# Kernel tuning notes

Measured on AMD Instinct MI355X. Metric: run time of the kernel, lower is better.

Reference implementation:

```python
import jax, jax.numpy as jnp
import numpy as np

KEEP_RATIO = 0.7

def setup_inputs() -> dict:
    key = jax.random.key(0)
    k1, k2, k3 = jax.random.split(key, 3)
    B, N, D = 4, 16384, 1024
    H = D // 4
    x = jax.random.normal(k1, (B, N, D), dtype=jnp.float32)
    W1 = jax.random.normal(k2, (D, H), dtype=jnp.float32) * (1.0 / np.sqrt(D))
    b1 = jnp.zeros((H,), dtype=jnp.float32)
    W2 = jax.random.normal(k3, (H, 1), dtype=jnp.float32) * (1.0 / np.sqrt(H))
    b2 = jnp.zeros((1,), dtype=jnp.float32)
    return {"x": x, "W1": W1, "b1": b1, "W2": W2, "b2": b2}

def reference(x, W1, b1, W2, b2):
    # x: [B, N, D]
    B, N, D = x.shape
    k = int(N * KEEP_RATIO)  # static under jit
    h = jax.nn.relu(jnp.einsum('bnd,dh->bnh', x, W1) + b1)
    scores = jax.nn.sigmoid(jnp.einsum('bnh,ho->bno', h, W2) + b2)  # [B, N, 1]
    score_values = scores[..., 0]  # [B, N]
    x_weighted = x * scores  # [B, N, D]
    _, top_k_indices = jax.lax.top_k(score_values, k)  # [B, k]
    top_k_indices = jnp.sort(top_k_indices, axis=1)
    x_kept = jnp.take_along_axis(x_weighted, top_k_indices[:, :, None], axis=1)  # [B, k, D]
    sparsity_loss = -jnp.mean(jnp.abs(score_values - 0.5))
    return x_kept, sparsity_loss
```

## Files before the change

### kernel.cpp

```cpp
#include <hip/hip_runtime.h>
#include <hip/hip_bf16.h>
#include <math.h>

#define N_TOK 16384
#define BATCH 4
#define DIM   1024
#define HID   256
#define KEEP  11468
#define MROWS 65536
#define BK    32
#define NKT   (DIM / BK)
#define DELTA 6e-3f
#define WCAP  4096
#define AP    40
#define ASLOT (128 * AP)
#define BSLOT (16 * 512)

typedef __attribute__((ext_vector_type(8))) short bf16x8;
typedef __attribute__((ext_vector_type(4))) float f32x4;

__device__ inline unsigned bf16_rne(float f) {
    unsigned u = __float_as_uint(f);
    return (u + 0x7FFFu + ((u >> 16) & 1u)) >> 16;
}

#define GLDS16(gp, lp) __builtin_amdgcn_global_load_lds( \
    (const __attribute__((address_space(1))) void*)(gp), \
    (__attribute__((address_space(3))) void*)(lp), 16, 0, 0)

__global__ __launch_bounds__(256) void prep_kernel(
    const float* __restrict__ W1, ushort* __restrict__ Wpk)
{
    const int kt = blockIdx.x;
    for (int idx = threadIdx.x; idx < 2048; idx += 256) {
        const int lane = idx & 63;
        const int g    = idx >> 6;
        const int h    = (g & 15) * 16 + (lane & 15);
        const int kb   = kt * 64 + (g >> 4) * 32 + (lane >> 4) * 8;
        ushort v[8];
#pragma unroll
        for (int j = 0; j < 8; ++j)
            v[j] = (ushort)bf16_rne(W1[(size_t)(kb + j) * HID + h]);
        *(uint4*)(Wpk + ((size_t)(kt * 32 + g) * 64 + lane) * 8) = *(uint4*)v;
    }
}

__global__ __launch_bounds__(512, 4) void score_mfma(
    const float* __restrict__ x, const ushort* __restrict__ Wpk,
    const float* __restrict__ b1, const float* __restrict__ W2,
    const float* __restrict__ b2, float* __restrict__ scores,
    float* __restrict__ partials)
{
    __shared__ ushort AsAll[3 * ASLOT];
    __shared__ ushort BsAll[3 * BSLOT];

    const int t    = threadIdx.x;
    const int lane = t & 63;
    const int w    = t >> 6;
    const int wr   = w >> 2;
    const int wc   = w & 3;
    const int l15  = lane & 15;
    const int lk   = lane >> 4;
    const size_t row0 = (size_t)blockIdx.x * 128;

    const int arow = t >> 2;
    const int aq   = t & 3;
    const float* xbase = x + (row0 + arow) * DIM + aq * 8;

    f32x4 acc[4][4];
#pragma unroll
    for (int rf = 0; rf < 4; ++rf)
#pragma unroll
        for (int cf = 0; cf < 4; ++cf) acc[rf][cf] = (f32x4){0.f, 0.f, 0.f, 0.f};

    float4 p0a, p0b, p1a, p1b;

#define ISSUEA(KT, PA, PB) { \
        const float4* xp = (const float4*)(xbase + (size_t)(KT) * BK); \
        PA = xp[0]; PB = xp[1]; }
#define CONVA(PA, PB, SLOT) { \
        ushort hb[8]; \
        hb[0] = (ushort)bf16_rne(PA.x); hb[1] = (ushort)bf16_rne(PA.y); \
        hb[2] = (ushort)bf16_rne(PA.z); hb[3] = (ushort)bf16_rne(PA.w); \
        hb[4] = (ushort)bf16_rne(PB.x); hb[5] = (ushort)bf16_rne(PB.y); \
        hb[6] = (ushort)bf16_rne(PB.z); hb[7] = (ushort)bf16_rne(PB.w); \
        *(uint4*)&AsAll[(SLOT) * ASLOT + arow * AP + aq * 8] = *(uint4*)&hb[0]; }
#define ISSUEB(KT, SLOT) { \
        _Pragma("unroll") \
        for (int i = 0; i < 2; ++i) { \
            const int g_ = w * 2 + i; \
            GLDS16(Wpk + (((size_t)(KT) * 16 + g_) * 64 + lane) * 8, \
                   &BsAll[(SLOT) * BSLOT + g_ * 512 + lane * 8]); \
        } }
#define COMPUTE(SLOT) { \
        bf16x8 Af[4]; \
        _Pragma("unroll") \
        for (int rf = 0; rf < 4; ++rf) { \
            const int row = wr * 64 + rf * 16 + l15; \
            Af[rf] = *(const bf16x8*)&AsAll[(SLOT) * ASLOT + row * AP + lk * 8]; \
        } \
        _Pragma("unroll") \
        for (int cf = 0; cf < 4; ++cf) { \
            const bf16x8 Bf = *(const bf16x8*)&BsAll[(SLOT) * BSLOT + (wc * 4 + cf) * 512 + lane * 8]; \
            acc[0][cf] = __builtin_amdgcn_mfma_f32_16x16x32_bf16(Af[0], Bf, acc[0][cf], 0, 0, 0); \
            acc[1][cf] = __builtin_amdgcn_mfma_f32_16x16x32_bf16(Af[1], Bf, acc[1][cf], 0, 0, 0); \
            acc[2][cf] = __builtin_amdgcn_mfma_f32_16x16x32_bf16(Af[2], Bf, acc[2][cf], 0, 0, 0); \
            acc[3][cf] = __builtin_amdgcn_mfma_f32_16x16x32_bf16(Af[3], Bf, acc[3][cf], 0, 0, 0); \
        } }

    ISSUEB(0, 0);
    ISSUEA(0, p0a, p0b);
    ISSUEA(1, p1a, p1b);
    CONVA(p0a, p0b, 0);
    asm volatile("s_waitcnt lgkmcnt(0)" ::: "memory");
    __builtin_amdgcn_s_barrier();
    __builtin_amdgcn_sched_barrier(0);

    for (int kt = 0; kt < NKT; ++kt) {
        if (kt < NKT - 2) {
            if ((kt & 1) == 0) { ISSUEA(kt + 2, p0a, p0b); }
            else               { ISSUEA(kt + 2, p1a, p1b); }
        }
        if (kt < NKT - 1) {
            const int s1 = (kt + 1) % 3;
            ISSUEB(kt + 1, s1);
            if ((kt & 1) == 0) { CONVA(p1a, p1b, s1); }
            else               { CONVA(p0a, p0b, s1); }
        }
        if (kt < NKT - 2)       asm volatile("s_waitcnt vmcnt(4)" ::: "memory");
        else if (kt == NKT - 2) asm volatile("s_waitcnt vmcnt(2)" ::: "memory");
        else                    asm volatile("s_waitcnt vmcnt(0)" ::: "memory");
        asm volatile("s_waitcnt lgkmcnt(0)" ::: "memory");
        __builtin_amdgcn_s_barrier();
        __builtin_amdgcn_sched_barrier(0);
        COMPUTE(kt % 3);
    }

    float* zb = (float*)&BsAll[0];
    float* rd = (float*)&BsAll[1024];
    float b1r[4], w2r[4];
#pragma unroll
    for (int cf = 0; cf < 4; ++cf) {
        const int col = wc * 64 + cf * 16 + l15;
        b1r[cf] = b1[col];
        w2r[cf] = W2[col];
    }
#pragma unroll
    for (int rf = 0; rf < 4; ++rf) {
#pragma unroll
        for (int j = 0; j < 4; ++j) {
            float z = 0.f;
#pragma unroll
            for (int cf = 0; cf < 4; ++cf)
                z = fmaf(fmaxf(acc[rf][cf][j] + b1r[cf], 0.f), w2r[cf], z);
            z += __shfl_xor(z, 1);
            z += __shfl_xor(z, 2);
            z += __shfl_xor(z, 4);
            z += __shfl_xor(z, 8);
            if (l15 == 0) zb[(wr * 64 + rf * 16 + lk * 4 + j) * 4 + wc] = z;
        }
    }
    __syncthreads();
    if (t < 128) {
        const float z = (zb[t * 4 + 0] + zb[t * 4 + 1]) + (zb[t * 4 + 2] + zb[t * 4 + 3]) + b2[0];
        const float s = 1.f / (1.f + expf(-z));
        scores[row0 + t] = s;
        rd[t] = fabsf(s - 0.5f);
    }
    __syncthreads();
    for (int off = 64; off > 0; off >>= 1) {
        if (t < off) rd[t] += rd[t + off];
        __syncthreads();
    }
    if (t == 0) partials[blockIdx.x] = rd[0];
}

__global__ __launch_bounds__(1024) void fixfind_kernel(
    const float* __restrict__ scores, int* __restrict__ winList,
    int* __restrict__ winCnt)
{
    const int b    = blockIdx.x;
    const int t    = threadIdx.x;
    const int lane = t & 63;
    const int wid  = t >> 6;
    __shared__ unsigned red[17];
    __shared__ unsigned wsum[16];

    float sv[16];
    unsigned bits[16];
    const float4* sp = (const float4*)(scores + (size_t)b * N_TOK + t * 16);
#pragma unroll
    for (int j = 0; j < 4; ++j) {
        const float4 v = sp[j];
        sv[j * 4 + 0] = v.x; sv[j * 4 + 1] = v.y;
        sv[j * 4 + 2] = v.z; sv[j * 4 + 3] = v.w;
    }
#pragma unroll
    for (int j = 0; j < 16; ++j) bits[j] = __float_as_uint(sv[j]);

    auto countGE = [&](unsigned v) -> unsigned {
        unsigned c = 0;
#pragma unroll
        for (int j = 0; j < 16; ++j) c += (bits[j] >= v) ? 1u : 0u;
        c += __shfl_xor(c, 32); c += __shfl_xor(c, 16); c += __shfl_xor(c, 8);
        c += __shfl_xor(c, 4);  c += __shfl_xor(c, 2);  c += __shfl_xor(c, 1);
        if (lane == 0) red[wid] = c;
        __syncthreads();
        if (wid == 0) {
            unsigned s = (lane < 16) ? red[lane] : 0u;
            s += __shfl_xor(s, 8); s += __shfl_xor(s, 4);
            s += __shfl_xor(s, 2); s += __shfl_xor(s, 1);
            if (lane == 0) red[16] = s;
        }
        __syncthreads();
        return red[16];
    };

    unsigned lo = 0u, hi = 0x40000000u;
    while (hi - lo > 1u) {
        const unsigned mid = (lo + hi) >> 1;
        if (countGE(mid) >= KEEP) lo = mid; else hi = mid;
    }
    const float sT = __uint_as_float(lo);

    int cnt = 0;
    bool inw[16];
#pragma unroll
    for (int j = 0; j < 16; ++j) {
        inw[j] = fabsf(sv[j] - sT) <= DELTA;
        cnt += inw[j] ? 1 : 0;
    }
    unsigned inc = (unsigned)cnt;
#pragma unroll
    for (int off = 1; off < 64; off <<= 1) {
        const unsigned n = __shfl_up(inc, off);
        if (lane >= off) inc += n;
    }
    const unsigned excl = inc - (unsigned)cnt;
    if (lane == 63) wsum[wid] = inc;
    __syncthreads();
    if (t == 0) {
        unsigned s = 0;
        for (int w = 0; w < 16; ++w) { const unsigned tmp = wsum[w]; wsum[w] = s; s += tmp; }
        winCnt[b] = (int)(s > WCAP ? WCAP : s);
    }
    __syncthreads();
    unsigned pos = wsum[wid] + excl;
#pragma unroll
    for (int j = 0; j < 16; ++j) {
        if (inw[j]) {
            if (pos < WCAP) winList[b * WCAP + pos] = t * 16 + j;
            ++pos;
        }
    }
}

__global__ __launch_bounds__(1024) void fix2_kernel(
    const float* __restrict__ x, const float* __restrict__ W1,
    const float* __restrict__ b1, const float* __restrict__ W2,
    const float* __restrict__ b2, float* __restrict__ scores,
    const int* __restrict__ winList, const int* __restrict__ winCnt)
{
    __shared__ float xrT[1024][8];
    __shared__ float part[4][8][256];
    __shared__ int rows[8];

    const int t = threadIdx.x;
    int c[4], cum[5];
    cum[0] = 0;
    for (int b = 0; b < 4; ++b) {
        int cc = winCnt[b];
        if (cc > WCAP) cc = WCAP;
        if (cc < 0) cc = 0;
        c[b] = cc;
        cum[b + 1] = cum[b] + ((cc + 7) >> 3);
    }
    for (int g = blockIdx.x; g < cum[4]; g += gridDim.x) {
        int b = 0;
        while (g >= cum[b + 1]) ++b;
        const int gi   = g - cum[b];
        const int nval = min(8, c[b] - gi * 8);
        if (t < 8)
            rows[t] = winList[b * WCAP + gi * 8 + (t < nval ? t : 0)];
        __syncthreads();
        {
            const int r = t >> 7, c0 = (t & 127) * 8;
            const float* xp = x + ((size_t)b * N_TOK + rows[r]) * DIM + c0;
            const float4 a = ((const float4*)xp)[0], bq = ((const float4*)xp)[1];
            xrT[c0 + 0][r] = a.x;  xrT[c0 + 1][r] = a.y;
            xrT[c0 + 2][r] = a.z;  xrT[c0 + 3][r] = a.w;
            xrT[c0 + 4][r] = bq.x; xrT[c0 + 5][r] = bq.y;
            xrT[c0 + 6][r] = bq.z; xrT[c0 + 7][r] = bq.w;
        }
        __syncthreads();
        const int h = t & 255, q = t >> 8;
        float a8[8];
#pragma unroll
        for (int r = 0; r < 8; ++r) a8[r] = 0.f;
        const int k0 = q * 256;
        for (int k = 0; k < 256; ++k) {
            const float wv = W1[(size_t)(k0 + k) * HID + h];
            const float4 xa = *(const float4*)&xrT[k0 + k][0];
            const float4 xb = *(const float4*)&xrT[k0 + k][4];
            a8[0] = fmaf(xa.x, wv, a8[0]); a8[1] = fmaf(xa.y, wv, a8[1]);
            a8[2] = fmaf(xa.z, wv, a8[2]); a8[3] = fmaf(xa.w, wv, a8[3]);
            a8[4] = fmaf(xb.x, wv, a8[4]); a8[5] = fmaf(xb.y, wv, a8[5]);
            a8[6] = fmaf(xb.z, wv, a8[6]); a8[7] = fmaf(xb.w, wv, a8[7]);
        }
#pragma unroll
        for (int r = 0; r < 8; ++r) part[q][r][h] = a8[r];
        __syncthreads();
        const int wid = t >> 6, lane = t & 63;
        if (wid < 8) {
            const int r = wid;
            float v = 0.f;
#pragma unroll
            for (int i = 0; i < 4; ++i) {
                const int hc = i * 64 + lane;
                float hv = (part[0][r][hc] + part[1][r][hc]) + (part[2][r][hc] + part[3][r][hc]);
                hv = fmaxf(hv + b1[hc], 0.f);
                v = fmaf(hv, W2[hc], v);
            }
            v += __shfl_xor(v, 32); v += __shfl_xor(v, 16); v += __shfl_xor(v, 8);
            v += __shfl_xor(v, 4);  v += __shfl_xor(v, 2);  v += __shfl_xor(v, 1);
            if (lane == 0 && r < nval)
                scores[(size_t)b * N_TOK + rows[r]] = 1.f / (1.f + expf(-(v + b2[0])));
        }
        __syncthreads();
    }
}

__global__ __launch_bounds__(1024) void select_kernel(
    const float* __restrict__ scores, int* __restrict__ idxList)
{
    const int b    = blockIdx.x;
    const int t    = threadIdx.x;
    const int lane = t & 63;
    const int wid  = t >> 6;
    __shared__ unsigned red[17];

    unsigned bits[16];
    const float4* sp = (const float4*)(scores + (size_t)b * N_TOK + t * 16);
#pragma unroll
    for (int j = 0; j < 4; ++j) {
        const float4 v = sp[j];
        bits[j * 4 + 0] = __float_as_uint(v.x);
        bits[j * 4 + 1] = __float_as_uint(v.y);
        bits[j * 4 + 2] = __float_as_uint(v.z);
        bits[j * 4 + 3] = __float_as_uint(v.w);
    }

    auto countGE = [&](unsigned v) -> unsigned {
        unsigned c = 0;
#pragma unroll
        for (int j = 0; j < 16; ++j) c += (bits[j] >= v) ? 1u : 0u;
        c += __shfl_xor(c, 32); c += __shfl_xor(c, 16); c += __shfl_xor(c, 8);
        c += __shfl_xor(c, 4);  c += __shfl_xor(c, 2);  c += __shfl_xor(c, 1);
        if (lane == 0) red[wid] = c;
        __syncthreads();
        if (wid == 0) {
            unsigned s = (lane < 16) ? red[lane] : 0u;
            s += __shfl_xor(s, 8); s += __shfl_xor(s, 4);
            s += __shfl_xor(s, 2); s += __shfl_xor(s, 1);
            if (lane == 0) red[16] = s;
        }
        __syncthreads();
        return red[16];
    };

    unsigned lo = 0u, hi = 0x40000000u;
    while (hi - lo > 1u) {
        const unsigned mid = (lo + hi) >> 1;
        if (countGE(mid) >= KEEP) lo = mid; else hi = mid;
    }
    const unsigned T    = lo;
    const unsigned cGT  = countGE(T + 1u);
    const unsigned need = KEEP - cGT;

    unsigned pre[16];
    unsigned run = 0;
#pragma unroll
    for (int j = 0; j < 16; ++j) {
        pre[j] = run;
        const unsigned gt = (bits[j] > T) ? 1u : 0u;
        const unsigned eq = (bits[j] == T) ? 1u : 0u;
        run += gt | (eq << 16);
    }
    unsigned inc = run;
#pragma unroll
    for (int off = 1; off < 64; off <<= 1) {
        const unsigned n = __shfl_up(inc, off);
        if (lane >= off) inc += n;
    }
    const unsigned waveExcl = inc - run;
    if (lane == 63) red[wid] = inc;
    __syncthreads();
    if (t == 0) {
        unsigned s = 0;
        for (int w = 0; w < 16; ++w) { const unsigned tmp = red[w]; red[w] = s; s += tmp; }
    }
    __syncthreads();
    const unsigned base = red[wid] + waveExcl;

#pragma unroll
    for (int j = 0; j < 16; ++j) {
        const unsigned pe    = base + pre[j];
        const unsigned tieR  = pe >> 16;
        const unsigned posGT = pe & 0xFFFFu;
        const bool gt = bits[j] > T;
        const bool eq = bits[j] == T;
        if (gt || (eq && tieR < need)) {
            const unsigned pos = posGT + (tieR < need ? tieR : need);
            idxList[(size_t)b * KEEP + pos] = t * 16 + j;
        }
    }
}

__global__ __launch_bounds__(256) void gather_kernel(
    const float* __restrict__ x, const float* __restrict__ scores,
    const int* __restrict__ idxList, float* __restrict__ out)
{
    const int t = threadIdx.x;
#pragma unroll
    for (int q = 0; q < 4; ++q) {
        const int orow = blockIdx.x * 4 + q;
        const int b    = orow / KEEP;
        const int idx  = idxList[orow];
        const float s  = scores[(size_t)b * N_TOK + idx];
        const float4 v = *(const float4*)(x + (((size_t)b * N_TOK + idx) << 10) + t * 4);
        float4 o;
        o.x = v.x * s; o.y = v.y * s; o.z = v.z * s; o.w = v.w * s;
        *(float4*)(out + ((size_t)orow << 10) + t * 4) = o;
    }
}

__global__ __launch_bounds__(256) void loss_kernel(
    const float* __restrict__ partials, float* __restrict__ outLoss)
{
    __shared__ float red[256];
    const int t = threadIdx.x;
    red[t] = partials[t] + partials[t + 256];
    __syncthreads();
    for (int off = 128; off > 0; off >>= 1) {
        if (t < off) red[t] += red[t + off];
        __syncthreads();
    }
    if (t == 0) outLoss[0] = -(red[0] / (float)MROWS);
}

extern "C" void kernel_launch(void* const* d_in, const int* in_sizes, int n_in,
                              void* d_out, int out_size, void* d_ws, size_t ws_size,
                              hipStream_t stream)
{
    const float* x  = (const float*)d_in[0];
    const float* W1 = (const float*)d_in[1];
    const float* b1 = (const float*)d_in[2];
    const float* W2 = (const float*)d_in[3];
    const float* b2 = (const float*)d_in[4];
    float* out = (float*)d_out;

    char* ws = (char*)d_ws;
    float* scores   = (float*)ws;
    float* partials = (float*)(ws + 262144);
    int*   idxList  = (int*)(ws + 266240);
    ushort* Wpk     = (ushort*)(ws + 458752);
    int*   winList  = (int*)(ws + 983040);
    int*   winCnt   = (int*)(ws + 1048576);

    prep_kernel<<<16, 256, 0, stream>>>(W1, Wpk);
    score_mfma<<<MROWS / 128, 512, 0, stream>>>(x, Wpk, b1, W2, b2, scores, partials);
    loss_kernel<<<1, 256, 0, stream>>>(partials, out + (size_t)BATCH * KEEP * DIM);
    fixfind_kernel<<<BATCH, 1024, 0, stream>>>(scores, winList, winCnt);
    fix2_kernel<<<256, 1024, 0, stream>>>(x, W1, b1, W2, b2, scores, winList, winCnt);
    select_kernel<<<BATCH, 1024, 0, stream>>>(scores, idxList);
    gather_kernel<<<KEEP, 256, 0, stream>>>(x, scores, idxList, out);
}
```

Measured before the change: 227.7 us.

## Replace bisection threshold search with three-pass radix histogram select

Swaps the 30-step binary search for the top-k threshold, where each step does a block-wide count with two barriers, for a radix select. The select builds a 16-bit high-digit histogram in shared memory with atomics, runs a suffix scan, then refines with two 8-bit histograms to get the exact threshold and the count above it. This cuts the number of block-wide barrier rounds in the fixfind and select kernels. In exchange it uses about 64KB of shared memory per block and adds shared-memory atomic contention, since the scores cluster into a few buckets.

```diff
diff --git a/kernel.cpp b/kernel.cpp
--- a/kernel.cpp
+++ b/kernel.cpp
@@ -27,6 +27,121 @@
 #define GLDS16(gp, lp) __builtin_amdgcn_global_load_lds( \
     (const __attribute__((address_space(1))) void*)(gp), \
     (__attribute__((address_space(3))) void*)(lp), 16, 0, 0)
+
+__device__ __forceinline__ void radix_thresh(
+    const unsigned bits[16], const int t, const int lane, const int wid,
+    unsigned* hist, unsigned* aux, unsigned& T, unsigned& cGT)
+{
+#pragma unroll
+    for (int i = 0; i < 16; ++i) hist[t * 16 + i] = 0u;
+    if (t == 0) hist[16384] = 0u;
+    __syncthreads();
+#pragma unroll
+    for (int j = 0; j < 16; ++j) atomicAdd(&hist[bits[j] >> 16], 1u);
+    __syncthreads();
+    unsigned loc[16];
+    unsigned s = 0;
+#pragma unroll
+    for (int i = 15; i >= 0; --i) { s += hist[t * 16 + i]; loc[i] = s; }
+    unsigned inc = s;
+#pragma unroll
+    for (int off = 1; off < 64; off <<= 1) {
+        const unsigned n = __shfl_down(inc, off);
+        if (lane + off < 64) inc += n;
+    }
+    if (lane == 0) aux[wid] = inc;
+    __syncthreads();
+    if (t == 0) {
+        unsigned run = 0;
+        for (int w = 15; w >= 0; --w) { const unsigned tmp = aux[w]; aux[w] = run; run += tmp; }
+    }
+    __syncthreads();
+    const unsigned above = aux[wid] + (inc - s);
+#pragma unroll
+    for (int i = 0; i < 16; ++i) hist[t * 16 + i] = loc[i] + above;
+    __syncthreads();
+#pragma unroll
+    for (int i = 0; i < 16; ++i) {
+        const int B = t * 16 + i;
+        if (hist[B] >= KEEP && hist[B + 1] < KEEP) {
+            aux[16] = (unsigned)B;
+            aux[17] = hist[B + 1];
+        }
+    }
+    __syncthreads();
+    const unsigned B1 = aux[16];
+    const unsigned base1 = aux[17];
+    __syncthreads();
+
+    if (t < 257) hist[t] = 0u;
+    __syncthreads();
+#pragma unroll
+    for (int j = 0; j < 16; ++j)
+        if ((bits[j] >> 16) == B1) atomicAdd(&hist[(bits[j] >> 8) & 0xFFu], 1u);
+    __syncthreads();
+    if (wid == 0) {
+        unsigned l4[4];
+        unsigned ss = 0;
+#pragma unroll
+        for (int i = 3; i >= 0; --i) { ss += hist[lane * 4 + i]; l4[i] = ss; }
+        unsigned inc2 = ss;
+#pragma unroll
+        for (int off = 1; off < 64; off <<= 1) {
+            const unsigned n = __shfl_down(inc2, off);
+            if (lane + off < 64) inc2 += n;
+        }
+        const unsigned abv = inc2 - ss;
+#pragma unroll
+        for (int i = 0; i < 4; ++i) hist[lane * 4 + i] = l4[i] + abv;
+        if (lane == 0) hist[256] = 0u;
+    }
+    __syncthreads();
+    if (t < 256) {
+        if (base1 + hist[t] >= KEEP && base1 + hist[t + 1] < KEEP) {
+            aux[18] = (unsigned)t;
+            aux[19] = base1 + hist[t + 1];
+        }
+    }
+    __syncthreads();
+    const unsigned b2 = aux[18];
+    const unsigned base2 = aux[19];
+    __syncthreads();
+
+    const unsigned pfx = (B1 << 8) | b2;
+    if (t < 257) hist[t] = 0u;
+    __syncthreads();
+#pragma unroll
+    for (int j = 0; j < 16; ++j)
+        if ((bits[j] >> 8) == pfx) atomicAdd(&hist[bits[j] & 0xFFu], 1u);
+    __syncthreads();
+    if (wid == 0) {
+        unsigned l4[4];
+        unsigned ss = 0;
+#pragma unroll
+        for (int i = 3; i >= 0; --i) { ss += hist[lane * 4 + i]; l4[i] = ss; }
+        unsigned inc2 = ss;
+#pragma unroll
+        for (int off = 1; off < 64; off <<= 1) {
+            const unsigned n = __shfl_down(inc2, off);
+            if (lane + off < 64) inc2 += n;
+        }
+        const unsigned abv = inc2 - ss;
+#pragma unroll
+        for (int i = 0; i < 4; ++i) hist[lane * 4 + i] = l4[i] + abv;
+        if (lane == 0) hist[256] = 0u;
+    }
+    __syncthreads();
+    if (t < 256) {
+        if (base2 + hist[t] >= KEEP && base2 + hist[t + 1] < KEEP) {
+            aux[20] = (unsigned)t;
+            aux[21] = base2 + hist[t + 1];
+        }
+    }
+    __syncthreads();
+    T   = (B1 << 16) | (b2 << 8) | aux[20];
+    cGT = aux[21];
+    __syncthreads();
+}
 
 __global__ __launch_bounds__(256) void prep_kernel(
     const float* __restrict__ W1, ushort* __restrict__ Wpk)
@@ -183,7 +298,8 @@
     const int t    = threadIdx.x;
     const int lane = t & 63;
     const int wid  = t >> 6;
-    __shared__ unsigned red[17];
+    __shared__ unsigned hist[16385];
+    __shared__ unsigned aux[24];
     __shared__ unsigned wsum[16];
 
     float sv[16];
@@ -198,30 +314,9 @@
 #pragma unroll
     for (int j = 0; j < 16; ++j) bits[j] = __float_as_uint(sv[j]);
 
-    auto countGE = [&](unsigned v) -> unsigned {
-        unsigned c = 0;
-#pragma unroll
-        for (int j = 0; j < 16; ++j) c += (bits[j] >= v) ? 1u : 0u;
-        c += __shfl_xor(c, 32); c += __shfl_xor(c, 16); c += __shfl_xor(c, 8);
-        c += __shfl_xor(c, 4);  c += __shfl_xor(c, 2);  c += __shfl_xor(c, 1);
-        if (lane == 0) red[wid] = c;
-        __syncthreads();
-        if (wid == 0) {
-            unsigned s = (lane < 16) ? red[lane] : 0u;
-            s += __shfl_xor(s, 8); s += __shfl_xor(s, 4);
-            s += __shfl_xor(s, 2); s += __shfl_xor(s, 1);
-            if (lane == 0) red[16] = s;
-        }
-        __syncthreads();
-        return red[16];
-    };
-
-    unsigned lo = 0u, hi = 0x40000000u;
-    while (hi - lo > 1u) {
-        const unsigned mid = (lo + hi) >> 1;
-        if (countGE(mid) >= KEEP) lo = mid; else hi = mid;
-    }
-    const float sT = __uint_as_float(lo);
+    unsigned T, cGT;
+    radix_thresh(bits, t, lane, wid, hist, aux, T, cGT);
+    const float sT = __uint_as_float(T);
 
     int cnt = 0;
     bool inw[16];
@@ -337,7 +432,9 @@
     const int t    = threadIdx.x;
     const int lane = t & 63;
     const int wid  = t >> 6;
-    __shared__ unsigned red[17];
+    __shared__ unsigned hist[16385];
+    __shared__ unsigned aux[24];
+    __shared__ unsigned wsum[16];
 
     unsigned bits[16];
     const float4* sp = (const float4*)(scores + (size_t)b * N_TOK + t * 16);
@@ -350,31 +447,8 @@
         bits[j * 4 + 3] = __float_as_uint(v.w);
     }
 
-    auto countGE = [&](unsigned v) -> unsigned {
-        unsigned c = 0;
-#pragma unroll
-        for (int j = 0; j < 16; ++j) c += (bits[j] >= v) ? 1u : 0u;
-        c += __shfl_xor(c, 32); c += __shfl_xor(c, 16); c += __shfl_xor(c, 8);
-        c += __shfl_xor(c, 4);  c += __shfl_xor(c, 2);  c += __shfl_xor(c, 1);
-        if (lane == 0) red[wid] = c;
-        __syncthreads();
-        if (wid == 0) {
-            unsigned s = (lane < 16) ? red[lane] : 0u;
-            s += __shfl_xor(s, 8); s += __shfl_xor(s, 4);
-            s += __shfl_xor(s, 2); s += __shfl_xor(s, 1);
-            if (lane == 0) red[16] = s;
-        }
-        __syncthreads();
-        return red[16];
-    };
-
-    unsigned lo = 0u, hi = 0x40000000u;
-    while (hi - lo > 1u) {
-        const unsigned mid = (lo + hi) >> 1;
-        if (countGE(mid) >= KEEP) lo = mid; else hi = mid;
-    }
-    const unsigned T    = lo;
-    const unsigned cGT  = countGE(T + 1u);
+    unsigned T, cGT;
+    radix_thresh(bits, t, lane, wid, hist, aux, T, cGT);
     const unsigned need = KEEP - cGT;
 
     unsigned pre[16];
@@ -393,14 +467,14 @@
         if (lane >= off) inc += n;
     }
     const unsigned waveExcl = inc - run;
-    if (lane == 63) red[wid] = inc;
+    if (lane == 63) wsum[wid] = inc;
     __syncthreads();
     if (t == 0) {
         unsigned s = 0;
-        for (int w = 0; w < 16; ++w) { const unsigned tmp = red[w]; red[w] = s; s += tmp; }
-    }
-    __syncthreads();
-    const unsigned base = red[wid] + waveExcl;
+        for (int w = 0; w < 16; ++w) { const unsigned tmp = wsum[w]; wsum[w] = s; s += tmp; }
+    }
+    __syncthreads();
+    const unsigned base = wsum[wid] + waveExcl;
 
 #pragma unroll
     for (int j = 0; j < 16; ++j) {
```

After: 203.9 us. 10.4% less time.
